# Performance work log

Measured on AMD Instinct MI355X. Metric: run time of the kernel, lower is better.

## Reference

```python
import jax, jax.numpy as jnp
import numpy as np


def _qrnn_forward(X, W, b):
    seq_len, batch, d = X.shape
    H = W.shape[0] // 3
    Y = jnp.einsum('sbd,hd->sbh', X, W) + b  # [S,B,3H]
    Z, F, O = jnp.split(Y, 3, axis=2)
    Z = jnp.tanh(Z)
    F = jax.nn.sigmoid(F)

    # ForgetMult with hidden_init=None: h_0 = f_0*z_0; h_t = f_t*z_t + (1-f_t)*h_{t-1}
    # Equivalent to scan from h_{-1} = 0.
    def step(h_prev, fz):
        f_t, z_t = fz
        h = f_t * z_t + (1.0 - f_t) * h_prev
        return h, h

    h0 = jnp.zeros((batch, H), dtype=X.dtype)
    _, C = jax.lax.scan(step, h0, (F, Z))  # [S,B,H]
    Hout = jax.nn.sigmoid(O) * C
    return Hout, C[-1:, :, :]


def setup_inputs() -> dict:
    key = jax.random.key(0)
    k1, k2, k3 = jax.random.split(key, 3)
    S, B, D, Hdim = 1024, 16, 1024, 1024
    X = jax.random.normal(k1, (S, B, D), dtype=jnp.float32)
    W = jax.random.normal(k2, (3 * Hdim, D), dtype=jnp.float32) * (1.0 / np.sqrt(D))
    b = jax.random.normal(k3, (3 * Hdim,), dtype=jnp.float32) * 0.01
    return {"X": X, "W": W, "b": b}


def reference(X, W, b):
    return _qrnn_forward(X, W, b)
```

## Files before the change

kernel.cpp:

```cpp
#include <hip/hip_runtime.h>
#include <hip/hip_bf16.h>
#include <stdint.h>

typedef __bf16 bf16x8 __attribute__((ext_vector_type(8)));
typedef float f32x4 __attribute__((ext_vector_type(4)));

constexpr int S = 1024, Bsz = 16, Hd = 1024;
constexpr int M = S * Bsz;
constexpr int N = 3 * Hd;
constexpr int K = 1024;
constexpr int BM = 128, BN = 128, BK = 32;
constexpr int NCH = 32, CS = S / NCH;
constexpr int BH = Bsz * Hd;

__device__ __forceinline__ float fast_sigmoid(float x) { return 1.0f / (1.0f + __expf(-x)); }
__device__ __forceinline__ float fast_tanh(float x) { return 2.0f / (1.0f + __expf(-2.0f * x)) - 1.0f; }

__device__ __forceinline__ void gld_lds16(const __bf16* g, __bf16* l) {
  __builtin_amdgcn_global_load_lds(
      (const __attribute__((address_space(1))) void*)g,
      (__attribute__((address_space(3))) void*)l,
      16, 0, 0);
}

__global__ void convert_f32_bf16(const float* __restrict__ src, __bf16* __restrict__ dst, int n8) {
  int i = blockIdx.x * blockDim.x + threadIdx.x;
  if (i >= n8) return;
  const float4* s4 = (const float4*)src;
  float4 a = s4[2 * i], b = s4[2 * i + 1];
  bf16x8 v;
  v[0] = (__bf16)a.x; v[1] = (__bf16)a.y; v[2] = (__bf16)a.z; v[3] = (__bf16)a.w;
  v[4] = (__bf16)b.x; v[5] = (__bf16)b.y; v[6] = (__bf16)b.z; v[7] = (__bf16)b.w;
  *((bf16x8*)dst + i) = v;
}

__global__ __launch_bounds__(256) void gemm_act(const __bf16* __restrict__ A,
                                                const __bf16* __restrict__ Bw,
                                                const float* __restrict__ bias,
                                                __bf16* __restrict__ Y) {
  __shared__ __align__(16) __bf16 As[BM * BK];
  __shared__ __align__(16) __bf16 Bs[BN * BK];
  const int t = threadIdx.x;
  const int lane = t & 63;
  const int wave = t >> 6;
  const int wm = wave >> 1, wn = wave & 1;
  const int tn = blockIdx.x % (N / BN);
  const int tm = blockIdx.x / (N / BN);
  const int m0 = tm * BM, n0 = tn * BN;
  const int lrow = lane & 15;
  const int quad = lane >> 4;

  const int srow = t >> 2;
  const int scw = t & 3;
  const __bf16* gA0 = A + (size_t)(m0 + srow) * K + scw * 8;
  const __bf16* gA1 = gA0 + (size_t)64 * K;
  const __bf16* gB0 = Bw + (size_t)(n0 + srow) * K + scw * 8;
  const __bf16* gB1 = gB0 + (size_t)64 * K;
  __bf16* lA0 = As + wave * 512;
  __bf16* lA1 = As + 2048 + wave * 512;
  __bf16* lB0 = Bs + wave * 512;
  __bf16* lB1 = Bs + 2048 + wave * 512;

  f32x4 acc[4][4] = {};

  for (int k0 = 0; k0 < K; k0 += BK) {
    __syncthreads();
    gld_lds16(gA0, lA0);
    gld_lds16(gA1, lA1);
    gld_lds16(gB0, lB0);
    gld_lds16(gB1, lB1);
    gA0 += BK; gA1 += BK; gB0 += BK; gB1 += BK;
    __syncthreads();

    bf16x8 af[4], bfr[4];
#pragma unroll
    for (int mi = 0; mi < 4; ++mi)
      af[mi] = *(const bf16x8*)(&As[(wm * 64 + mi * 16 + lrow) * BK + quad * 8]);
#pragma unroll
    for (int ni = 0; ni < 4; ++ni)
      bfr[ni] = *(const bf16x8*)(&Bs[(wn * 64 + ni * 16 + lrow) * BK + quad * 8]);
#pragma unroll
    for (int mi = 0; mi < 4; ++mi)
#pragma unroll
      for (int ni = 0; ni < 4; ++ni)
        acc[mi][ni] = __builtin_amdgcn_mfma_f32_16x16x32_bf16(af[mi], bfr[ni], acc[mi][ni], 0, 0, 0);
  }

#pragma unroll
  for (int ni = 0; ni < 4; ++ni) {
    int col = n0 + wn * 64 + ni * 16 + lrow;
    float bv = bias[col];
    bool is_tanh = (col < Hd);
#pragma unroll
    for (int mi = 0; mi < 4; ++mi) {
#pragma unroll
      for (int r = 0; r < 4; ++r) {
        int m = m0 + wm * 64 + mi * 16 + quad * 4 + r;
        float y = acc[mi][ni][r] + bv;
        float v = is_tanh ? fast_tanh(y) : fast_sigmoid(y);
        Y[(size_t)m * N + col] = (__bf16)v;
      }
    }
  }
}

__global__ __launch_bounds__(256) void scan_pass1(const __bf16* __restrict__ Y,
                                                  float* __restrict__ Ac,
                                                  float* __restrict__ Bc) {
  int tid = blockIdx.x * 256 + threadIdx.x;
  int c = tid >> 11;
  int r = tid & 2047;
  int bh0 = r << 3;
  int b = bh0 >> 10, h0 = bh0 & (Hd - 1);
  const size_t sstep = (size_t)Bsz * N;
  size_t base0 = (size_t)b * N + h0 + (size_t)(c * CS) * sstep;
  float A[8], Bv[8];
#pragma unroll
  for (int v = 0; v < 8; ++v) { A[v] = 1.0f; Bv[v] = 0.0f; }
#pragma unroll 2
  for (int j0 = 0; j0 < CS; j0 += 8) {
    bf16x8 zv[8], fv[8];
#pragma unroll
    for (int j = 0; j < 8; ++j) {
      size_t base = base0 + (size_t)(j0 + j) * sstep;
      zv[j] = *(const bf16x8*)(Y + base);
      fv[j] = *(const bf16x8*)(Y + base + Hd);
    }
#pragma unroll
    for (int j = 0; j < 8; ++j) {
#pragma unroll
      for (int v = 0; v < 8; ++v) {
        float z = (float)zv[j][v], f = (float)fv[j][v];
        float a = 1.0f - f;
        Bv[v] = fmaf(a, Bv[v], f * z);
        A[v] *= a;
      }
    }
  }
  int ob = c * BH + bh0;
  f32x4 a0, a1, b0, b1;
#pragma unroll
  for (int v = 0; v < 4; ++v) { a0[v] = A[v]; a1[v] = A[v + 4]; b0[v] = Bv[v]; b1[v] = Bv[v + 4]; }
  *(f32x4*)(Ac + ob) = a0;
  *(f32x4*)(Ac + ob + 4) = a1;
  *(f32x4*)(Bc + ob) = b0;
  *(f32x4*)(Bc + ob + 4) = b1;
}

__global__ __launch_bounds__(256) void scan_pass2(const float* __restrict__ Ac,
                                                  const float* __restrict__ Bc,
                                                  float* __restrict__ hin,
                                                  float* __restrict__ clast) {
  int bh = blockIdx.x * 256 + threadIdx.x;
  float h = 0.0f;
#pragma unroll 4
  for (int c = 0; c < NCH; ++c) {
    hin[c * BH + bh] = h;
    h = fmaf(Ac[c * BH + bh], h, Bc[c * BH + bh]);
  }
  clast[bh] = h;
}

__global__ __launch_bounds__(256) void scan_pass3(const __bf16* __restrict__ Y,
                                                  const float* __restrict__ hin,
                                                  float* __restrict__ hout) {
  int tid = blockIdx.x * 256 + threadIdx.x;
  int c = tid >> 11;
  int r = tid & 2047;
  int bh0 = r << 3;
  int b = bh0 >> 10, h0 = bh0 & (Hd - 1);
  const size_t sstep = (size_t)Bsz * N;
  size_t base0 = (size_t)b * N + h0 + (size_t)(c * CS) * sstep;
  size_t obase0 = (size_t)b * Hd + h0 + (size_t)(c * CS) * BH;
  float hp[8];
  {
    f32x4 h04 = *(const f32x4*)(hin + c * BH + bh0);
    f32x4 h14 = *(const f32x4*)(hin + c * BH + bh0 + 4);
#pragma unroll
    for (int v = 0; v < 4; ++v) { hp[v] = h04[v]; hp[v + 4] = h14[v]; }
  }
  for (int j0 = 0; j0 < CS; j0 += 8) {
    bf16x8 zv[8], fv[8], ov[8];
#pragma unroll
    for (int j = 0; j < 8; ++j) {
      size_t base = base0 + (size_t)(j0 + j) * sstep;
      zv[j] = *(const bf16x8*)(Y + base);
      fv[j] = *(const bf16x8*)(Y + base + Hd);
      ov[j] = *(const bf16x8*)(Y + base + 2 * Hd);
    }
#pragma unroll
    for (int j = 0; j < 8; ++j) {
      f32x4 o0, o1;
#pragma unroll
      for (int v = 0; v < 8; ++v) {
        float z = (float)zv[j][v], f = (float)fv[j][v], o = (float)ov[j][v];
        hp[v] = fmaf(f, z - hp[v], hp[v]);
        float out = o * hp[v];
        if (v < 4) o0[v] = out; else o1[v - 4] = out;
      }
      size_t ob = obase0 + (size_t)(j0 + j) * BH;
      *(f32x4*)(hout + ob) = o0;
      *(f32x4*)(hout + ob + 4) = o1;
    }
  }
}

extern "C" void kernel_launch(void* const* d_in, const int* in_sizes, int n_in,
                              void* d_out, int out_size, void* d_ws, size_t ws_size,
                              hipStream_t stream) {
  const float* X = (const float*)d_in[0];
  const float* W = (const float*)d_in[1];
  const float* bias = (const float*)d_in[2];
  float* out = (float*)d_out;

  char* ws = (char*)d_ws;
  __bf16* Xb = (__bf16*)ws;
  __bf16* Wb = (__bf16*)(ws + 33554432);
  __bf16* Yv = (__bf16*)(ws + 39845888);
  float* Ac = (float*)(ws + 39845888 + 100663296);
  float* Bc = Ac + NCH * BH;
  float* hin = Bc + NCH * BH;

  convert_f32_bf16<<<8192, 256, 0, stream>>>(X, Xb, 2097152);
  convert_f32_bf16<<<1536, 256, 0, stream>>>(W, Wb, 393216);

  dim3 ggrid((M / BM) * (N / BN));
  dim3 vgrid(NCH * BH / 8 / 256);
  gemm_act<<<ggrid, 256, 0, stream>>>(Xb, Wb, bias, Yv);
  scan_pass1<<<vgrid, 256, 0, stream>>>(Yv, Ac, Bc);
  scan_pass2<<<BH / 256, 256, 0, stream>>>(Ac, Bc, hin, out + 16777216);
  scan_pass3<<<vgrid, 256, 0, stream>>>(Yv, hin, out);
}
```

Measured before the change: 307.1 us.

## Stage GEMM epilogue through LDS, widen BK, swizzle blocks, double scan chunks

The GEMM epilogue now writes activated results into a padded shared-memory tile and then stores them to Y as coalesced 16-byte rows. Before, each lane issued scattered 2-byte stores. The K tile doubles to 64, with two MFMA sub-steps per barrier pair, and the block index is permuted so that concurrently running blocks share cache lines. The scan uses 64 chunks instead of 32 and fully unrolls its inner loops, which adds parallelism in pass1 and pass3 but doubles the carry arrays in workspace and lengthens pass2. The extra LDS and larger unrolls may raise register pressure and reduce occupancy.

```diff
diff --git a/kernel.cpp b/kernel.cpp
--- a/kernel.cpp
+++ b/kernel.cpp
@@ -9,9 +9,10 @@
 constexpr int M = S * Bsz;
 constexpr int N = 3 * Hd;
 constexpr int K = 1024;
-constexpr int BM = 128, BN = 128, BK = 32;
-constexpr int NCH = 32, CS = S / NCH;
+constexpr int BM = 128, BN = 128, BK = 64;
+constexpr int NCH = 64, CS = S / NCH;
 constexpr int BH = Bsz * Hd;
+constexpr int EP = 136;
 
 __device__ __forceinline__ float fast_sigmoid(float x) { return 1.0f / (1.0f + __expf(-x)); }
 __device__ __forceinline__ float fast_tanh(float x) { return 2.0f / (1.0f + __expf(-2.0f * x)) - 1.0f; }
@@ -38,69 +39,83 @@
                                                 const __bf16* __restrict__ Bw,
                                                 const float* __restrict__ bias,
                                                 __bf16* __restrict__ Y) {
-  __shared__ __align__(16) __bf16 As[BM * BK];
-  __shared__ __align__(16) __bf16 Bs[BN * BK];
+  __shared__ __align__(16) __bf16 smem[BM * EP];
+  __bf16* As = smem;
+  __bf16* Bs = smem + BM * BK;
   const int t = threadIdx.x;
   const int lane = t & 63;
   const int wave = t >> 6;
   const int wm = wave >> 1, wn = wave & 1;
-  const int tn = blockIdx.x % (N / BN);
-  const int tm = blockIdx.x / (N / BN);
+  const int bid = blockIdx.x;
+  const int swz = (bid & 7) * (3072 / 8) + (bid >> 3);
+  const int tn = swz % (N / BN);
+  const int tm = swz / (N / BN);
   const int m0 = tm * BM, n0 = tn * BN;
   const int lrow = lane & 15;
   const int quad = lane >> 4;
 
-  const int srow = t >> 2;
-  const int scw = t & 3;
-  const __bf16* gA0 = A + (size_t)(m0 + srow) * K + scw * 8;
-  const __bf16* gA1 = gA0 + (size_t)64 * K;
-  const __bf16* gB0 = Bw + (size_t)(n0 + srow) * K + scw * 8;
-  const __bf16* gB1 = gB0 + (size_t)64 * K;
-  __bf16* lA0 = As + wave * 512;
-  __bf16* lA1 = As + 2048 + wave * 512;
-  __bf16* lB0 = Bs + wave * 512;
-  __bf16* lB1 = Bs + 2048 + wave * 512;
+  const int srow = t >> 3;
+  const int scol = (t & 7) * 8;
+  const __bf16* gA = A + (size_t)(m0 + srow) * K + scol;
+  const __bf16* gB = Bw + (size_t)(n0 + srow) * K + scol;
+  __bf16* lA = As + wave * 512;
+  __bf16* lB = Bs + wave * 512;
 
   f32x4 acc[4][4] = {};
 
   for (int k0 = 0; k0 < K; k0 += BK) {
     __syncthreads();
-    gld_lds16(gA0, lA0);
-    gld_lds16(gA1, lA1);
-    gld_lds16(gB0, lB0);
-    gld_lds16(gB1, lB1);
-    gA0 += BK; gA1 += BK; gB0 += BK; gB1 += BK;
+#pragma unroll
+    for (int i = 0; i < 4; ++i) {
+      gld_lds16(gA + (size_t)i * 32 * K, lA + i * 2048);
+      gld_lds16(gB + (size_t)i * 32 * K, lB + i * 2048);
+    }
+    gA += BK; gB += BK;
     __syncthreads();
 
-    bf16x8 af[4], bfr[4];
-#pragma unroll
-    for (int mi = 0; mi < 4; ++mi)
-      af[mi] = *(const bf16x8*)(&As[(wm * 64 + mi * 16 + lrow) * BK + quad * 8]);
-#pragma unroll
-    for (int ni = 0; ni < 4; ++ni)
-      bfr[ni] = *(const bf16x8*)(&Bs[(wn * 64 + ni * 16 + lrow) * BK + quad * 8]);
-#pragma unroll
-    for (int mi = 0; mi < 4; ++mi)
+#pragma unroll
+    for (int kk = 0; kk < 2; ++kk) {
+      bf16x8 af[4], bfr[4];
+#pragma unroll
+      for (int mi = 0; mi < 4; ++mi)
+        af[mi] = *(const bf16x8*)(&As[(wm * 64 + mi * 16 + lrow) * BK + kk * 32 + quad * 8]);
 #pragma unroll
       for (int ni = 0; ni < 4; ++ni)
-        acc[mi][ni] = __builtin_amdgcn_mfma_f32_16x16x32_bf16(af[mi], bfr[ni], acc[mi][ni], 0, 0, 0);
-  }
-
+        bfr[ni] = *(const bf16x8*)(&Bs[(wn * 64 + ni * 16 + lrow) * BK + kk * 32 + quad * 8]);
+#pragma unroll
+      for (int mi = 0; mi < 4; ++mi)
+#pragma unroll
+        for (int ni = 0; ni < 4; ++ni)
+          acc[mi][ni] = __builtin_amdgcn_mfma_f32_16x16x32_bf16(af[mi], bfr[ni], acc[mi][ni], 0, 0, 0);
+    }
+  }
+
+  __syncthreads();
 #pragma unroll
   for (int ni = 0; ni < 4; ++ni) {
-    int col = n0 + wn * 64 + ni * 16 + lrow;
+    int colL = wn * 64 + ni * 16 + lrow;
+    int col = n0 + colL;
     float bv = bias[col];
     bool is_tanh = (col < Hd);
 #pragma unroll
     for (int mi = 0; mi < 4; ++mi) {
 #pragma unroll
       for (int r = 0; r < 4; ++r) {
-        int m = m0 + wm * 64 + mi * 16 + quad * 4 + r;
+        int rowL = wm * 64 + mi * 16 + quad * 4 + r;
         float y = acc[mi][ni][r] + bv;
         float v = is_tanh ? fast_tanh(y) : fast_sigmoid(y);
-        Y[(size_t)m * N + col] = (__bf16)v;
+        smem[rowL * EP + colL] = (__bf16)v;
       }
     }
+  }
+  __syncthreads();
+#pragma unroll
+  for (int it = 0; it < 8; ++it) {
+    int slot = it * 256 + t;
+    int rowL = slot >> 4;
+    int cw = slot & 15;
+    bf16x8 vv = *(const bf16x8*)(&smem[rowL * EP + cw * 8]);
+    *(bf16x8*)(&Y[(size_t)(m0 + rowL) * N + n0 + cw * 8]) = vv;
   }
 }
 
@@ -117,7 +132,7 @@
   float A[8], Bv[8];
 #pragma unroll
   for (int v = 0; v < 8; ++v) { A[v] = 1.0f; Bv[v] = 0.0f; }
-#pragma unroll 2
+#pragma unroll
   for (int j0 = 0; j0 < CS; j0 += 8) {
     bf16x8 zv[8], fv[8];
 #pragma unroll
@@ -153,7 +168,7 @@
                                                   float* __restrict__ clast) {
   int bh = blockIdx.x * 256 + threadIdx.x;
   float h = 0.0f;
-#pragma unroll 4
+#pragma unroll 8
   for (int c = 0; c < NCH; ++c) {
     hin[c * BH + bh] = h;
     h = fmaf(Ac[c * BH + bh], h, Bc[c * BH + bh]);
@@ -179,6 +194,7 @@
 #pragma unroll
     for (int v = 0; v < 4; ++v) { hp[v] = h04[v]; hp[v + 4] = h14[v]; }
   }
+#pragma unroll
   for (int j0 = 0; j0 < CS; j0 += 8) {
     bf16x8 zv[8], fv[8], ov[8];
 #pragma unroll
```

After: 345.2 us. 1.12x slower.

## Stage GEMM epilogue through LDS for coalesced stores, merge converts, double scan chunks

Applied to the files above, without the earlier changes.

The GEMM epilogue now writes activated bf16 values into a padded LDS tile and then stores full 16-byte rows to Y, replacing scattered 2-byte global stores. The two f32-to-bf16 conversion launches are merged into one kernel. The scan is split into 64 chunks instead of 32, giving the scan passes more parallelism, and their loops are fully unrolled. In exchange, the GEMM uses more LDS per block (which may lower occupancy), the carry pass over chunks gets longer, and the intermediate chunk buffers grow.

```diff
diff --git a/kernel.cpp b/kernel.cpp
--- a/kernel.cpp
+++ b/kernel.cpp
@@ -10,8 +10,9 @@
 constexpr int N = 3 * Hd;
 constexpr int K = 1024;
 constexpr int BM = 128, BN = 128, BK = 32;
-constexpr int NCH = 32, CS = S / NCH;
+constexpr int NCH = 64, CS = S / NCH;
 constexpr int BH = Bsz * Hd;
+constexpr int EP = 136;
 
 __device__ __forceinline__ float fast_sigmoid(float x) { return 1.0f / (1.0f + __expf(-x)); }
 __device__ __forceinline__ float fast_tanh(float x) { return 2.0f / (1.0f + __expf(-2.0f * x)) - 1.0f; }
@@ -23,23 +24,27 @@
       16, 0, 0);
 }
 
-__global__ void convert_f32_bf16(const float* __restrict__ src, __bf16* __restrict__ dst, int n8) {
+__global__ void convert_all(const float* __restrict__ X, const float* __restrict__ W,
+                            __bf16* __restrict__ Xb, __bf16* __restrict__ Wb) {
   int i = blockIdx.x * blockDim.x + threadIdx.x;
-  if (i >= n8) return;
+  const float* src; __bf16* dst; int idx;
+  if (i < 2097152) { src = X; dst = Xb; idx = i; }
+  else             { src = W; dst = Wb; idx = i - 2097152; }
   const float4* s4 = (const float4*)src;
-  float4 a = s4[2 * i], b = s4[2 * i + 1];
+  float4 a = s4[2 * idx], b = s4[2 * idx + 1];
   bf16x8 v;
   v[0] = (__bf16)a.x; v[1] = (__bf16)a.y; v[2] = (__bf16)a.z; v[3] = (__bf16)a.w;
   v[4] = (__bf16)b.x; v[5] = (__bf16)b.y; v[6] = (__bf16)b.z; v[7] = (__bf16)b.w;
-  *((bf16x8*)dst + i) = v;
+  *((bf16x8*)dst + idx) = v;
 }
 
 __global__ __launch_bounds__(256) void gemm_act(const __bf16* __restrict__ A,
                                                 const __bf16* __restrict__ Bw,
                                                 const float* __restrict__ bias,
                                                 __bf16* __restrict__ Y) {
-  __shared__ __align__(16) __bf16 As[BM * BK];
-  __shared__ __align__(16) __bf16 Bs[BN * BK];
+  __shared__ __align__(16) __bf16 smem[BM * EP];
+  __bf16* As = smem;
+  __bf16* Bs = smem + 4096;
   const int t = threadIdx.x;
   const int lane = t & 63;
   const int wave = t >> 6;
@@ -86,21 +91,32 @@
         acc[mi][ni] = __builtin_amdgcn_mfma_f32_16x16x32_bf16(af[mi], bfr[ni], acc[mi][ni], 0, 0, 0);
   }
 
+  __syncthreads();
 #pragma unroll
   for (int ni = 0; ni < 4; ++ni) {
-    int col = n0 + wn * 64 + ni * 16 + lrow;
+    int colL = wn * 64 + ni * 16 + lrow;
+    int col = n0 + colL;
     float bv = bias[col];
     bool is_tanh = (col < Hd);
 #pragma unroll
     for (int mi = 0; mi < 4; ++mi) {
 #pragma unroll
       for (int r = 0; r < 4; ++r) {
-        int m = m0 + wm * 64 + mi * 16 + quad * 4 + r;
+        int rowL = wm * 64 + mi * 16 + quad * 4 + r;
         float y = acc[mi][ni][r] + bv;
         float v = is_tanh ? fast_tanh(y) : fast_sigmoid(y);
-        Y[(size_t)m * N + col] = (__bf16)v;
+        smem[rowL * EP + colL] = (__bf16)v;
       }
     }
+  }
+  __syncthreads();
+#pragma unroll
+  for (int it = 0; it < 8; ++it) {
+    int slot = it * 256 + t;
+    int rowL = slot >> 4;
+    int cw = slot & 15;
+    bf16x8 vv = *(const bf16x8*)(&smem[rowL * EP + cw * 8]);
+    *(bf16x8*)(&Y[(size_t)(m0 + rowL) * N + n0 + cw * 8]) = vv;
   }
 }
 
@@ -117,7 +133,7 @@
   float A[8], Bv[8];
 #pragma unroll
   for (int v = 0; v < 8; ++v) { A[v] = 1.0f; Bv[v] = 0.0f; }
-#pragma unroll 2
+#pragma unroll
   for (int j0 = 0; j0 < CS; j0 += 8) {
     bf16x8 zv[8], fv[8];
 #pragma unroll
@@ -153,7 +169,7 @@
                                                   float* __restrict__ clast) {
   int bh = blockIdx.x * 256 + threadIdx.x;
   float h = 0.0f;
-#pragma unroll 4
+#pragma unroll 8
   for (int c = 0; c < NCH; ++c) {
     hin[c * BH + bh] = h;
     h = fmaf(Ac[c * BH + bh], h, Bc[c * BH + bh]);
@@ -179,6 +195,7 @@
 #pragma unroll
     for (int v = 0; v < 4; ++v) { hp[v] = h04[v]; hp[v + 4] = h14[v]; }
   }
+#pragma unroll
   for (int j0 = 0; j0 < CS; j0 += 8) {
     bf16x8 zv[8], fv[8], ov[8];
 #pragma unroll
@@ -221,8 +238,7 @@
   float* Bc = Ac + NCH * BH;
   float* hin = Bc + NCH * BH;
 
-  convert_f32_bf16<<<8192, 256, 0, stream>>>(X, Xb, 2097152);
-  convert_f32_bf16<<<1536, 256, 0, stream>>>(W, Wb, 393216);
+  convert_all<<<9728, 256, 0, stream>>>(X, W, Xb, Wb);
 
   dim3 ggrid((M / BM) * (N / BN));
   dim3 vgrid(NCH * BH / 8 / 256);
```

After: 310.1 us. No clear change (+1.0%).
